# Kernel optimization log

Measured on AMD Instinct MI355X. Metric: run time of the kernel, lower is better.

The kernel has to match this reference:

```python
import jax, jax.numpy as jnp
import numpy as np
import math

D_MODEL = 512
N_HEADS = 8
D_FF = 2048
EPS = 1e-5

def _layernorm(x, g, b):
    m = jnp.mean(x, axis=-1, keepdims=True)
    v = jnp.var(x, axis=-1, keepdims=True)
    return (x - m) * jax.lax.rsqrt(v + EPS) * g + b

def setup_inputs() -> dict:
    key = jax.random.key(0)
    ks = jax.random.split(key, 8)
    d, dff = D_MODEL, D_FF
    s = lambda fan: 1.0 / math.sqrt(fan)
    return {
        "x": jax.random.normal(ks[0], (4, 2048, d), dtype=jnp.float32),
        "w_qkv": jax.random.normal(ks[1], (d, 3 * d), dtype=jnp.float32) * s(d),
        "b_qkv": jnp.zeros((3 * d,), dtype=jnp.float32),
        "w1": jax.random.normal(ks[2], (d, dff), dtype=jnp.float32) * s(d),
        "b1": jnp.zeros((dff,), dtype=jnp.float32),
        "w2": jax.random.normal(ks[3], (dff, d), dtype=jnp.float32) * s(dff),
        "b2": jnp.zeros((d,), dtype=jnp.float32),
        "g1": jnp.ones((d,), dtype=jnp.float32),
        "be1": jnp.zeros((d,), dtype=jnp.float32),
        "g2": jnp.ones((d,), dtype=jnp.float32),
        "be2": jnp.zeros((d,), dtype=jnp.float32),
    }

def reference(x, w_qkv, b_qkv, w1, b1, w2, b2, g1, be1, g2, be2):
    B, L, d = x.shape
    H = N_HEADS
    hd = d // H
    # Faithful to original: scale = 1/sqrt(hd), scores = qk / scale = qk * sqrt(hd)
    inv_scale = math.sqrt(hd)
    qkv = x @ w_qkv + b_qkv            # [B, L, 3d]
    q, k, v = jnp.split(qkv, 3, axis=-1)
    split_heads = lambda t: t.reshape(B, L, H, hd).transpose(0, 2, 1, 3)  # [B,H,L,hd]
    q, k, v = map(split_heads, (q, k, v))
    scores = jnp.einsum('bhqd,bhkd->bhqk', q, k) * inv_scale
    attn = jax.nn.softmax(scores, axis=-1)
    out = jnp.einsum('bhqk,bhkd->bhqd', attn, v)
    out = out.transpose(0, 2, 1, 3).reshape(B, L, d)
    x = _layernorm(x + out, g1, be1)
    ff = jax.nn.relu(x @ w1 + b1) @ w2 + b2
    return _layernorm(x + ff, g2, be2)
```

## Files before the change

### kernel.cpp

```cpp
#include <hip/hip_runtime.h>

typedef _Float16 f16;
typedef _Float16 f16x4 __attribute__((ext_vector_type(4)));
typedef _Float16 f16x8 __attribute__((ext_vector_type(8)));
typedef float    f32x4 __attribute__((ext_vector_type(4)));
typedef float    f32x16 __attribute__((ext_vector_type(16)));
typedef unsigned int u32x4 __attribute__((ext_vector_type(4)));

#define QK_SCALE 11.5416528f

__device__ __forceinline__ void g2l16(const void* g, void* l) {
  __builtin_amdgcn_global_load_lds(
      (__attribute__((address_space(1))) const unsigned int*)g,
      (__attribute__((address_space(3))) unsigned int*)l, 16, 0, 0);
}

__device__ __forceinline__ f32x4 mfma16(f16x8 a, f16x8 b, f32x4 c) {
  return __builtin_amdgcn_mfma_f32_16x16x32_f16(a, b, c, 0, 0, 0);
}
__device__ __forceinline__ f32x16 mfma32(f16x8 a, f16x8 b, f32x16 c) {
  return __builtin_amdgcn_mfma_f32_32x32x16_f16(a, b, c, 0, 0, 0);
}
__device__ __forceinline__ unsigned pkrtz(float a, float b) {
  auto t = __builtin_amdgcn_cvt_pkrtz(a, b);
  return *(unsigned*)&t;
}
__device__ __forceinline__ void swap32(unsigned& a, unsigned& b) {
  asm volatile("v_permlane32_swap_b32 %0, %1" : "+v"(a), "+v"(b));
}

__device__ __forceinline__ int swz64(int row, int c) { return row * 64 + ((c ^ (row & 7)) << 3); }
__device__ __forceinline__ int swz32(int row, int c) { return row * 32 + ((c ^ ((row >> 1) & 3)) << 3); }

__global__ __launch_bounds__(256) void k_split(const float* __restrict__ in,
                                               f16* __restrict__ hi, f16* __restrict__ lo, int n4) {
  int i = blockIdx.x * 256 + threadIdx.x;
  if (i >= n4) return;
  f32x4 v = ((const f32x4*)in)[i];
  f16x4 h, l;
#pragma unroll
  for (int j = 0; j < 4; ++j) {
    f16 hv = (f16)v[j];
    h[j] = hv;
    l[j] = (f16)(v[j] - (float)hv);
  }
  ((f16x4*)hi)[i] = h;
  ((f16x4*)lo)[i] = l;
}

template <bool WLO>
__global__ __launch_bounds__(256) void k_transpose_split(const float* __restrict__ in, int K, int N,
                                                         f16* __restrict__ oh, f16* __restrict__ ol) {
  __shared__ float t[32][33];
  const int tx = threadIdx.x, ty = threadIdx.y;
  const int n0 = blockIdx.x * 32, k0 = blockIdx.y * 32;
#pragma unroll
  for (int j = 0; j < 4; ++j)
    t[ty + j * 8][tx] = in[(size_t)(k0 + ty + j * 8) * N + n0 + tx];
  __syncthreads();
#pragma unroll
  for (int j = 0; j < 4; ++j) {
    float v = t[tx][ty + j * 8];
    f16 hv = (f16)v;
    size_t o = (size_t)(n0 + ty + j * 8) * K + k0 + tx;
    oh[o] = hv;
    if (WLO) ol[o] = (f16)(v - (float)hv);
  }
}

template <int EPI, bool SPLIT>
__global__ __launch_bounds__(256, SPLIT ? 2 : 3) void k_gemm(
    const f16* __restrict__ Ah, const f16* __restrict__ Al,
    const f16* __restrict__ Bh, const f16* __restrict__ Bl,
    const float* __restrict__ bias,
    float* __restrict__ outF, float* __restrict__ outF2, f16* __restrict__ outH,
    f16* __restrict__ oqh, f16* __restrict__ oql,
    f16* __restrict__ okh, f16* __restrict__ ovT,
    int M, int N, int K, int ks) {
  constexpr int NB = SPLIT ? 2 : 1;
  __shared__ f16 As[NB][128 * 32];
  __shared__ f16 Bs[NB][128 * 32];

  const int tid = threadIdx.x;
  const int bm = blockIdx.x, bn = blockIdx.y;
  const int bnc = (EPI == 3) ? (bn & 3) : bn;
  const int half = (EPI == 3) ? (bn >> 2) : 0;
  const int hoff = half * 1024;
  const int w = tid >> 6, lane = tid & 63;
  const int wr = w >> 1, wc = w & 1;
  const int lrow = lane & 15, lgrp = lane >> 4;

  const bool useLo = SPLIT && !(EPI == 0 && bn >= 4);

  f32x4 acc[4][4] = {};

  const int nkt = K >> 5;
  for (int kt = 0; kt < nkt; ++kt) {
    __syncthreads();
    const int kk = kt << 5;
#pragma unroll
    for (int c = 0; c < 2; ++c) {
      const int i = tid + (c << 8);
      const int row = i >> 2;
      const int gch = ((i & 3) ^ ((i >> 3) & 3)) << 3;
      const size_t aoff = (size_t)(bm * 128 + row) * ks + hoff + kk + gch;
      const size_t boff = (size_t)(bnc * 128 + row) * ks + hoff + kk + gch;
      g2l16(Ah + aoff, &As[0][i * 8]);
      g2l16(Bh + boff, &Bs[0][i * 8]);
      if (SPLIT)
        if (useLo) {
          g2l16(Al + aoff, &As[1][i * 8]);
          g2l16(Bl + boff, &Bs[1][i * 8]);
        }
    }
    __syncthreads();

    f16x8 a0[4], a1[4], b0[4], b1[4];
#pragma unroll
    for (int mf = 0; mf < 4; ++mf) {
      const int off = swz32(wr * 64 + mf * 16 + lrow, lgrp);
      a0[mf] = *(const f16x8*)&As[0][off];
      if (SPLIT)
        if (useLo) a1[mf] = *(const f16x8*)&As[SPLIT ? 1 : 0][off];
    }
#pragma unroll
    for (int nf = 0; nf < 4; ++nf) {
      const int off = swz32(wc * 64 + nf * 16 + lrow, lgrp);
      b0[nf] = *(const f16x8*)&Bs[0][off];
      if (SPLIT)
        if (useLo) b1[nf] = *(const f16x8*)&Bs[SPLIT ? 1 : 0][off];
    }
#pragma unroll
    for (int mf = 0; mf < 4; ++mf)
#pragma unroll
      for (int nf = 0; nf < 4; ++nf) {
        acc[mf][nf] = mfma16(a0[mf], b0[nf], acc[mf][nf]);
        if (SPLIT)
          if (useLo) {
            acc[mf][nf] = mfma16(a0[mf], b1[nf], acc[mf][nf]);
            acc[mf][nf] = mfma16(a1[mf], b0[nf], acc[mf][nf]);
          }
      }
  }

  const int rowbase = bm * 128 + wr * 64 + lgrp * 4;
  const int colbase = bnc * 128 + wc * 64 + lrow;
#pragma unroll
  for (int mf = 0; mf < 4; ++mf) {
#pragma unroll
    for (int nf = 0; nf < 4; ++nf) {
      const int gc = colbase + nf * 16;
      const float bv = (EPI == 3 && half) ? 0.f : bias[gc];
#pragma unroll
      for (int r = 0; r < 4; ++r) {
        const int gr = rowbase + mf * 16 + r;
        const float val = acc[mf][nf][r] + bv;
        if (EPI == 0) {
          const int bb = gr >> 11, tok = gr & 2047;
          const int kind = gc >> 9, hh = (gc >> 6) & 7, dd = gc & 63;
          const size_t bhp = (size_t)((bb << 3) + hh);
          const size_t qidx = (bhp * 2048 + tok) * 64 + dd;
          if (kind == 0) {
            const float sv = val * QK_SCALE;
            const f16 hv = (f16)sv;
            oqh[qidx] = hv; oql[qidx] = (f16)(sv - (float)hv);
          } else if (kind == 1) {
            okh[qidx] = (f16)val;
          } else {
            ovT[(bhp * 64 + dd) * 2048 + tok] = (f16)val;
          }
        } else if (EPI == 1) {
          outH[(size_t)gr * N + gc] = (f16)fmaxf(val, 0.f);
        } else if (EPI == 2) {
          outF[(size_t)gr * N + gc] = val;
        } else {
          float* o = half ? outF2 : outF;
          o[(size_t)gr * N + gc] = val;
        }
      }
    }
  }
}

__global__ __launch_bounds__(256, 2) void k_attn(
    const f16* __restrict__ Qh, const f16* __restrict__ Ql,
    const f16* __restrict__ Kh, const f16* __restrict__ Vt,
    f16* __restrict__ out) {
  __shared__ f16 sK[4][64 * 64], sV[4][64 * 64];

  const int tid = threadIdx.x;
  const int wg = (blockIdx.x & 7) * 64 + (blockIdx.x >> 3);
  const int bh = wg >> 4, qt = wg & 15;
  const int w = tid >> 6, lane = tid & 63;
  const int lh = lane & 31, hh = lane >> 5;

  const int qrow = qt * 128 + w * 32 + lh;
  const size_t qoff = ((size_t)bh * 2048 + qrow) * 64;
  f16x8 qh8[4], ql8[4];
#pragma unroll
  for (int d = 0; d < 4; ++d) {
    const size_t o = qoff + d * 16 + hh * 8;
    qh8[d] = *(const f16x8*)(Qh + o);
    ql8[d] = *(const f16x8*)(Ql + o);
  }

  auto stage = [&](int b, int kt) {
    const size_t koff = ((size_t)bh * 2048 + (size_t)kt * 64) * 64;
    const size_t voff = (size_t)bh * 64 * 2048 + (size_t)kt * 64;
#pragma unroll
    for (int c = 0; c < 2; ++c) {
      const int i = tid + (c << 8);
      const int row = i >> 3;
      const int gch = ((i & 7) ^ (row & 7)) << 3;
      g2l16(Kh + koff + (size_t)row * 64 + gch, &sK[b][i * 8]);
      g2l16(Vt + voff + (size_t)row * 2048 + gch, &sV[b][i * 8]);
    }
  };

  stage(0, 0);
  stage(1, 1);
  stage(2, 2);

  float m_run = -3e38f;
  float l_run = 0.f;
  f32x16 oacc[2] = {};
  const f32x16 kZero = {};
  f32x16 sA[2] = {}, sB[2] = {};

  auto qk = [&](f32x16 (&s)[2], int bi) {
    __builtin_amdgcn_s_setprio(1);
    {
      const f16x8 k0 = *(const f16x8*)&sK[bi][swz64(lh, hh)];
      const f16x8 k1 = *(const f16x8*)&sK[bi][swz64(32 + lh, hh)];
      s[0] = mfma32(k0, qh8[0], kZero);
      s[0] = mfma32(k0, ql8[0], s[0]);
      s[1] = mfma32(k1, qh8[0], kZero);
      s[1] = mfma32(k1, ql8[0], s[1]);
    }
#pragma unroll
    for (int d = 1; d < 4; ++d) {
      const f16x8 k0 = *(const f16x8*)&sK[bi][swz64(lh, d * 2 + hh)];
      const f16x8 k1 = *(const f16x8*)&sK[bi][swz64(32 + lh, d * 2 + hh)];
      s[0] = mfma32(k0, qh8[d], s[0]);
      s[0] = mfma32(k0, ql8[d], s[0]);
      s[1] = mfma32(k1, qh8[d], s[1]);
      s[1] = mfma32(k1, ql8[d], s[1]);
    }
    __builtin_amdgcn_s_setprio(0);
  };

  auto sm_pv = [&](f32x16 (&s)[2], int bi) {
    float mt = s[0][0];
#pragma unroll
    for (int r = 0; r < 16; ++r) { mt = fmaxf(mt, s[0][r]); mt = fmaxf(mt, s[1][r]); }
    mt = fmaxf(mt, __shfl_xor(mt, 32, 64));
    float mcur = m_run;
    if (!__all(mt <= mcur + 8.0f)) {
      const float mnew = fmaxf(mcur, mt);
      const float corr = __builtin_amdgcn_exp2f(mcur - mnew);
      m_run = mnew;
      l_run *= corr;
      oacc[0] = oacc[0] * corr;
      oacc[1] = oacc[1] * corr;
      mcur = mnew;
    }
    float ps = 0.f;
    unsigned pk0[8], pk1[8];
#pragma unroll
    for (int i = 0; i < 8; ++i) {
      const float a0 = __builtin_amdgcn_exp2f(s[0][2 * i] - mcur);
      const float a1 = __builtin_amdgcn_exp2f(s[0][2 * i + 1] - mcur);
      const float b0 = __builtin_amdgcn_exp2f(s[1][2 * i] - mcur);
      const float b1 = __builtin_amdgcn_exp2f(s[1][2 * i + 1] - mcur);
      ps += (a0 + a1) + (b0 + b1);
      pk0[i] = pkrtz(a0, a1);
      pk1[i] = pkrtz(b0, b1);
    }
    ps += __shfl_xor(ps, 32, 64);
    l_run += ps;

    swap32(pk0[0], pk0[2]); swap32(pk0[1], pk0[3]);
    swap32(pk0[4], pk0[6]); swap32(pk0[5], pk0[7]);
    swap32(pk1[0], pk1[2]); swap32(pk1[1], pk1[3]);
    swap32(pk1[4], pk1[6]); swap32(pk1[5], pk1[7]);

    u32x4 pbu[4];
    pbu[0] = (u32x4){pk0[0], pk0[1], pk0[2], pk0[3]};
    pbu[1] = (u32x4){pk0[4], pk0[5], pk0[6], pk0[7]};
    pbu[2] = (u32x4){pk1[0], pk1[1], pk1[2], pk1[3]};
    pbu[3] = (u32x4){pk1[4], pk1[5], pk1[6], pk1[7]};

    __builtin_amdgcn_s_setprio(1);
#pragma unroll
    for (int s2 = 0; s2 < 4; ++s2) {
      const f16x8 pb = *(const f16x8*)&pbu[s2];
#pragma unroll
      for (int db = 0; db < 2; ++db) {
        const f16x8 v = *(const f16x8*)&sV[bi][swz64(db * 32 + lh, s2 * 2 + hh)];
        oacc[db] = mfma32(v, pb, oacc[db]);
      }
    }
    __builtin_amdgcn_s_setprio(0);
  };

  auto endwait = [&](int t) {
    if (t < 29) {
      asm volatile("s_waitcnt vmcnt(4)" ::: "memory");
    } else {
      asm volatile("s_waitcnt vmcnt(0)" ::: "memory");
    }
    __builtin_amdgcn_sched_barrier(0);
    __builtin_amdgcn_s_barrier();
    __builtin_amdgcn_sched_barrier(0);
  };

  asm volatile("s_waitcnt vmcnt(4)" ::: "memory");
  __builtin_amdgcn_sched_barrier(0);
  __builtin_amdgcn_s_barrier();
  __builtin_amdgcn_sched_barrier(0);
  qk(sA, 0);

  for (int t = 0; t < 32; t += 2) {
    {
      if (t + 1 < 32) qk(sB, (t + 1) & 3);
      if (t + 3 < 32) stage((t + 3) & 3, t + 3);
      sm_pv(sA, t & 3);
      if (t + 1 < 32) endwait(t);
    }
    if (t + 1 < 32) {
      if (t + 2 < 32) qk(sA, (t + 2) & 3);
      if (t + 4 < 32) stage((t + 4) & 3, t + 4);
      sm_pv(sB, (t + 1) & 3);
      if (t + 2 < 32) endwait(t + 1);
    }
  }

  const int b = bh >> 3, hd = bh & 7;
  const float inv = 1.0f / l_run;
  const int trow = b * 2048 + qt * 128 + w * 32 + lh;
  f16* po = out + (size_t)trow * 512 + hd * 64;
#pragma unroll
  for (int db = 0; db < 2; ++db)
#pragma unroll
    for (int rq = 0; rq < 4; ++rq) {
      f16x4 o;
#pragma unroll
      for (int j = 0; j < 4; ++j) o[j] = (f16)(oacc[db][rq * 4 + j] * inv);
      *(f16x4*)(po + db * 32 + rq * 8 + hh * 4) = o;
    }
}

__global__ __launch_bounds__(256) void k_ln1(const float* __restrict__ X, const f16* __restrict__ R,
                                             const float* __restrict__ g, const float* __restrict__ be,
                                             f16* __restrict__ outH) {
  const int row = blockIdx.x * 4 + (threadIdx.x >> 6);
  const int t = threadIdx.x & 63;
  const size_t base = (size_t)row * 512 + t * 8;
  f32x4 x0 = *(const f32x4*)(X + base);
  f32x4 x1 = *(const f32x4*)(X + base + 4);
  const f16x8 r = *(const f16x8*)(R + base);
#pragma unroll
  for (int j = 0; j < 4; ++j) { x0[j] += (float)r[j]; x1[j] += (float)r[j + 4]; }
  float s = 0.f, ss = 0.f;
#pragma unroll
  for (int j = 0; j < 4; ++j) { s += x0[j] + x1[j]; ss += x0[j] * x0[j] + x1[j] * x1[j]; }
#pragma unroll
  for (int o = 32; o; o >>= 1) {
    s += __shfl_xor(s, o, 64);
    ss += __shfl_xor(ss, o, 64);
  }
  const float mean = s * (1.f / 512.f);
  const float var = ss * (1.f / 512.f) - mean * mean;
  const float rs = rsqrtf(var + 1e-5f);
  f32x4 g0 = *(const f32x4*)(g + t * 8);
  f32x4 g1v = *(const f32x4*)(g + t * 8 + 4);
  f32x4 b0 = *(const f32x4*)(be + t * 8);
  f32x4 b1 = *(const f32x4*)(be + t * 8 + 4);
  f16x8 hx;
#pragma unroll
  for (int j = 0; j < 4; ++j) {
    hx[j] = (f16)((x0[j] - mean) * rs * g0[j] + b0[j]);
    hx[j + 4] = (f16)((x1[j] - mean) * rs * g1v[j] + b1[j]);
  }
  *(f16x8*)(outH + base) = hx;
}

__global__ __launch_bounds__(256) void k_ln2(const f16* __restrict__ Xh,
                                             const float* __restrict__ R0, const float* __restrict__ R1,
                                             const float* __restrict__ g, const float* __restrict__ be,
                                             float* __restrict__ out) {
  const int row = blockIdx.x * 4 + (threadIdx.x >> 6);
  const int t = threadIdx.x & 63;
  const size_t base = (size_t)row * 512 + t * 8;
  const f16x8 xv = *(const f16x8*)(Xh + base);
  f32x4 r00 = *(const f32x4*)(R0 + base);
  f32x4 r01 = *(const f32x4*)(R0 + base + 4);
  f32x4 r10 = *(const f32x4*)(R1 + base);
  f32x4 r11 = *(const f32x4*)(R1 + base + 4);
  f32x4 x0, x1;
#pragma unroll
  for (int j = 0; j < 4; ++j) {
    x0[j] = (float)xv[j] + r00[j] + r10[j];
    x1[j] = (float)xv[j + 4] + r01[j] + r11[j];
  }
  float s = 0.f, ss = 0.f;
#pragma unroll
  for (int j = 0; j < 4; ++j) { s += x0[j] + x1[j]; ss += x0[j] * x0[j] + x1[j] * x1[j]; }
#pragma unroll
  for (int o = 32; o; o >>= 1) {
    s += __shfl_xor(s, o, 64);
    ss += __shfl_xor(ss, o, 64);
  }
  const float mean = s * (1.f / 512.f);
  const float var = ss * (1.f / 512.f) - mean * mean;
  const float rs = rsqrtf(var + 1e-5f);
  f32x4 g0 = *(const f32x4*)(g + t * 8);
  f32x4 g1v = *(const f32x4*)(g + t * 8 + 4);
  f32x4 b0 = *(const f32x4*)(be + t * 8);
  f32x4 b1 = *(const f32x4*)(be + t * 8 + 4);
  f32x4 y0 = (x0 - mean) * rs * g0 + b0;
  f32x4 y1 = (x1 - mean) * rs * g1v + b1;
  *(f32x4*)(out + base) = y0;
  *(f32x4*)(out + base + 4) = y1;
}

extern "C" void kernel_launch(void* const* d_in, const int* in_sizes, int n_in,
                              void* d_out, int out_size, void* d_ws, size_t ws_size,
                              hipStream_t stream) {
  (void)in_sizes; (void)n_in; (void)out_size;
  const float* x = (const float*)d_in[0];
  const float* w_qkv = (const float*)d_in[1];
  const float* b_qkv = (const float*)d_in[2];
  const float* w1 = (const float*)d_in[3];
  const float* b1 = (const float*)d_in[4];
  const float* w2 = (const float*)d_in[5];
  const float* b2 = (const float*)d_in[6];
  const float* g1 = (const float*)d_in[7];
  const float* be1 = (const float*)d_in[8];
  const float* g2 = (const float*)d_in[9];
  const float* be2 = (const float*)d_in[10];
  float* out = (float*)d_out;

  char* p = (char*)d_ws;
  auto take = [&](size_t bytes) {
    char* r = p;
    p += (bytes + 255) & ~(size_t)255;
    return r;
  };
  f16* xh = (f16*)take(8192ull * 512 * 2);
  f16* xl = (f16*)take(8192ull * 512 * 2);
  f16* wqkvTh = (f16*)take(1536ull * 512 * 2);
  f16* wqkvTl = (f16*)take(1536ull * 512 * 2);
  f16* w1T = (f16*)take(2048ull * 512 * 2);
  f16* w2T = (f16*)take(512ull * 2048 * 2);
  f16* qh = (f16*)take(32ull * 2048 * 64 * 2);
  f16* ql = (f16*)take(32ull * 2048 * 64 * 2);
  f16* kh = (f16*)take(32ull * 2048 * 64 * 2);
  f16* vT = (f16*)take(32ull * 64 * 2048 * 2);
  f16* attnH = (f16*)take(8192ull * 512 * 2);
  f16* x1h = (f16*)take(8192ull * 512 * 2);
  float* ffb0 = (float*)take(8192ull * 512 * 4);
  float* ffb1 = (float*)take(8192ull * 512 * 4);
  f16* hbuf = qh;

  if ((size_t)(p - (char*)d_ws) > ws_size) return;

  dim3 tb(32, 8);
  k_split<<<4096, 256, 0, stream>>>(x, xh, xl, 8192 * 512 / 4);
  k_transpose_split<true><<<dim3(1536 / 32, 512 / 32), tb, 0, stream>>>(w_qkv, 512, 1536, wqkvTh, wqkvTl);
  k_transpose_split<false><<<dim3(2048 / 32, 512 / 32), tb, 0, stream>>>(w1, 512, 2048, w1T, nullptr);
  k_transpose_split<false><<<dim3(512 / 32, 2048 / 32), tb, 0, stream>>>(w2, 2048, 512, w2T, nullptr);

  k_gemm<0, true><<<dim3(64, 12), 256, 0, stream>>>(xh, xl, wqkvTh, wqkvTl, b_qkv,
                                                    nullptr, nullptr, nullptr, qh, ql, kh, vT,
                                                    8192, 1536, 512, 512);
  k_attn<<<512, 256, 0, stream>>>(qh, ql, kh, vT, attnH);
  k_ln1<<<2048, 256, 0, stream>>>(x, attnH, g1, be1, x1h);
  k_gemm<1, false><<<dim3(64, 16), 256, 0, stream>>>(x1h, nullptr, w1T, nullptr, b1,
                                                     nullptr, nullptr, hbuf, nullptr, nullptr, nullptr, nullptr,
                                                     8192, 2048, 512, 512);
  k_gemm<3, false><<<dim3(64, 8), 256, 0, stream>>>(hbuf, nullptr, w2T, nullptr, b2,
                                                    ffb0, ffb1, nullptr, nullptr, nullptr, nullptr, nullptr,
                                                    8192, 512, 1024, 2048);
  k_ln2<<<2048, 256, 0, stream>>>(x1h, ffb0, ffb1, g2, be2, out);
}
```

Before: 179.2 us.

## Multi-buffer GEMM LDS staging, restructure attention prefetch, store FFN partials in fp16

After: 198.7 us. +10.9%, slower.

```diff
diff --git a/kernel.cpp b/kernel.cpp
--- a/kernel.cpp
+++ b/kernel.cpp
@@ -29,6 +29,14 @@
   asm volatile("v_permlane32_swap_b32 %0, %1" : "+v"(a), "+v"(b));
 }
 
+#define WAIT_BARRIER(N)                                        \
+  do {                                                         \
+    asm volatile("s_waitcnt vmcnt(" #N ")" ::: "memory");      \
+    __builtin_amdgcn_sched_barrier(0);                         \
+    __builtin_amdgcn_s_barrier();                              \
+    __builtin_amdgcn_sched_barrier(0);                         \
+  } while (0)
+
 __device__ __forceinline__ int swz64(int row, int c) { return row * 64 + ((c ^ (row & 7)) << 3); }
 __device__ __forceinline__ int swz32(int row, int c) { return row * 32 + ((c ^ ((row >> 1) & 3)) << 3); }
 
@@ -73,13 +81,14 @@
     const f16* __restrict__ Ah, const f16* __restrict__ Al,
     const f16* __restrict__ Bh, const f16* __restrict__ Bl,
     const float* __restrict__ bias,
-    float* __restrict__ outF, float* __restrict__ outF2, f16* __restrict__ outH,
+    f16* __restrict__ outH, f16* __restrict__ outH2,
     f16* __restrict__ oqh, f16* __restrict__ oql,
     f16* __restrict__ okh, f16* __restrict__ ovT,
     int M, int N, int K, int ks) {
+  constexpr int NBUF = SPLIT ? 2 : 3;
   constexpr int NB = SPLIT ? 2 : 1;
-  __shared__ f16 As[NB][128 * 32];
-  __shared__ f16 Bs[NB][128 * 32];
+  __shared__ f16 As[NBUF][NB][128 * 32];
+  __shared__ f16 Bs[NBUF][NB][128 * 32];
 
   const int tid = threadIdx.x;
   const int bm = blockIdx.x, bn = blockIdx.y;
@@ -94,9 +103,7 @@
 
   f32x4 acc[4][4] = {};
 
-  const int nkt = K >> 5;
-  for (int kt = 0; kt < nkt; ++kt) {
-    __syncthreads();
+  auto stg = [&](int bf, int kt) {
     const int kk = kt << 5;
 #pragma unroll
     for (int c = 0; c < 2; ++c) {
@@ -105,30 +112,31 @@
       const int gch = ((i & 3) ^ ((i >> 3) & 3)) << 3;
       const size_t aoff = (size_t)(bm * 128 + row) * ks + hoff + kk + gch;
       const size_t boff = (size_t)(bnc * 128 + row) * ks + hoff + kk + gch;
-      g2l16(Ah + aoff, &As[0][i * 8]);
-      g2l16(Bh + boff, &Bs[0][i * 8]);
+      g2l16(Ah + aoff, &As[bf][0][i * 8]);
+      g2l16(Bh + boff, &Bs[bf][0][i * 8]);
       if (SPLIT)
         if (useLo) {
-          g2l16(Al + aoff, &As[1][i * 8]);
-          g2l16(Bl + boff, &Bs[1][i * 8]);
+          g2l16(Al + aoff, &As[bf][1][i * 8]);
+          g2l16(Bl + boff, &Bs[bf][1][i * 8]);
         }
     }
-    __syncthreads();
-
+  };
+
+  auto compute = [&](int bf) {
     f16x8 a0[4], a1[4], b0[4], b1[4];
 #pragma unroll
     for (int mf = 0; mf < 4; ++mf) {
       const int off = swz32(wr * 64 + mf * 16 + lrow, lgrp);
-      a0[mf] = *(const f16x8*)&As[0][off];
+      a0[mf] = *(const f16x8*)&As[bf][0][off];
       if (SPLIT)
-        if (useLo) a1[mf] = *(const f16x8*)&As[SPLIT ? 1 : 0][off];
+        if (useLo) a1[mf] = *(const f16x8*)&As[bf][SPLIT ? 1 : 0][off];
     }
 #pragma unroll
     for (int nf = 0; nf < 4; ++nf) {
       const int off = swz32(wc * 64 + nf * 16 + lrow, lgrp);
-      b0[nf] = *(const f16x8*)&Bs[0][off];
+      b0[nf] = *(const f16x8*)&Bs[bf][0][off];
       if (SPLIT)
-        if (useLo) b1[nf] = *(const f16x8*)&Bs[SPLIT ? 1 : 0][off];
+        if (useLo) b1[nf] = *(const f16x8*)&Bs[bf][SPLIT ? 1 : 0][off];
     }
 #pragma unroll
     for (int mf = 0; mf < 4; ++mf)
@@ -141,6 +149,32 @@
             acc[mf][nf] = mfma16(a1[mf], b0[nf], acc[mf][nf]);
           }
       }
+  };
+
+  const int nkt = K >> 5;
+  if constexpr (!SPLIT) {
+    stg(0, 0);
+    stg(1, 1);
+    WAIT_BARRIER(4);
+    for (int kt = 0; kt < nkt; ++kt) {
+      const int cur = kt % 3;
+      const bool more2 = (kt + 2 < nkt);
+      if (more2) stg((kt + 2) % 3, kt + 2);
+      compute(cur);
+      if (kt + 1 < nkt) {
+        if (more2) WAIT_BARRIER(4);
+        else       WAIT_BARRIER(0);
+      }
+    }
+  } else {
+    stg(0, 0);
+    WAIT_BARRIER(0);
+    for (int kt = 0; kt < nkt; ++kt) {
+      const int cur = kt & 1;
+      if (kt + 1 < nkt) stg(cur ^ 1, kt + 1);
+      compute(cur);
+      if (kt + 1 < nkt) WAIT_BARRIER(0);
+    }
   }
 
   const int rowbase = bm * 128 + wr * 64 + lgrp * 4;
@@ -171,11 +205,9 @@
           }
         } else if (EPI == 1) {
           outH[(size_t)gr * N + gc] = (f16)fmaxf(val, 0.f);
-        } else if (EPI == 2) {
-          outF[(size_t)gr * N + gc] = val;
         } else {
-          float* o = half ? outF2 : outF;
-          o[(size_t)gr * N + gc] = val;
+          f16* o = half ? outH2 : outH;
+          o[(size_t)gr * N + gc] = (f16)val;
         }
       }
     }
@@ -219,7 +251,6 @@
 
   stage(0, 0);
   stage(1, 1);
-  stage(2, 2);
 
   float m_run = -3e38f;
   float l_run = 0.f;
@@ -303,35 +334,20 @@
     __builtin_amdgcn_s_setprio(0);
   };
 
-  auto endwait = [&](int t) {
-    if (t < 29) {
-      asm volatile("s_waitcnt vmcnt(4)" ::: "memory");
-    } else {
-      asm volatile("s_waitcnt vmcnt(0)" ::: "memory");
-    }
-    __builtin_amdgcn_sched_barrier(0);
-    __builtin_amdgcn_s_barrier();
-    __builtin_amdgcn_sched_barrier(0);
-  };
-
-  asm volatile("s_waitcnt vmcnt(4)" ::: "memory");
-  __builtin_amdgcn_sched_barrier(0);
-  __builtin_amdgcn_s_barrier();
-  __builtin_amdgcn_sched_barrier(0);
+  WAIT_BARRIER(0);
   qk(sA, 0);
 
   for (int t = 0; t < 32; t += 2) {
-    {
-      if (t + 1 < 32) qk(sB, (t + 1) & 3);
-      if (t + 3 < 32) stage((t + 3) & 3, t + 3);
-      sm_pv(sA, t & 3);
-      if (t + 1 < 32) endwait(t);
-    }
-    if (t + 1 < 32) {
-      if (t + 2 < 32) qk(sA, (t + 2) & 3);
-      if (t + 4 < 32) stage((t + 4) & 3, t + 4);
-      sm_pv(sB, (t + 1) & 3);
-      if (t + 2 < 32) endwait(t + 1);
+    if (t + 2 < 32) {
+      stage((t + 2) & 3, t + 2);
+      stage((t + 3) & 3, t + 3);
+    }
+    qk(sB, (t + 1) & 3);
+    sm_pv(sA, t & 3);
+    sm_pv(sB, (t + 1) & 3);
+    if (t + 2 < 32) {
+      WAIT_BARRIER(0);
+      qk(sA, (t + 2) & 3);
     }
   }
 
@@ -386,22 +402,20 @@
 }
 
 __global__ __launch_bounds__(256) void k_ln2(const f16* __restrict__ Xh,
-                                             const float* __restrict__ R0, const float* __restrict__ R1,
+                                             const f16* __restrict__ R0, const f16* __restrict__ R1,
                                              const float* __restrict__ g, const float* __restrict__ be,
                                              float* __restrict__ out) {
   const int row = blockIdx.x * 4 + (threadIdx.x >> 6);
   const int t = threadIdx.x & 63;
   const size_t base = (size_t)row * 512 + t * 8;
   const f16x8 xv = *(const f16x8*)(Xh + base);
-  f32x4 r00 = *(const f32x4*)(R0 + base);
-  f32x4 r01 = *(const f32x4*)(R0 + base + 4);
-  f32x4 r10 = *(const f32x4*)(R1 + base);
-  f32x4 r11 = *(const f32x4*)(R1 + base + 4);
+  const f16x8 r0 = *(const f16x8*)(R0 + base);
+  const f16x8 r1 = *(const f16x8*)(R1 + base);
   f32x4 x0, x1;
 #pragma unroll
   for (int j = 0; j < 4; ++j) {
-    x0[j] = (float)xv[j] + r00[j] + r10[j];
-    x1[j] = (float)xv[j + 4] + r01[j] + r11[j];
+    x0[j] = (float)xv[j] + (float)r0[j] + (float)r1[j];
+    x1[j] = (float)xv[j + 4] + (float)r0[j + 4] + (float)r1[j + 4];
   }
   float s = 0.f, ss = 0.f;
 #pragma unroll
@@ -459,8 +473,8 @@
   f16* vT = (f16*)take(32ull * 64 * 2048 * 2);
   f16* attnH = (f16*)take(8192ull * 512 * 2);
   f16* x1h = (f16*)take(8192ull * 512 * 2);
-  float* ffb0 = (float*)take(8192ull * 512 * 4);
-  float* ffb1 = (float*)take(8192ull * 512 * 4);
+  f16* ffb0 = (f16*)take(8192ull * 512 * 2);
+  f16* ffb1 = (f16*)take(8192ull * 512 * 2);
   f16* hbuf = qh;
 
   if ((size_t)(p - (char*)d_ws) > ws_size) return;
@@ -472,15 +486,15 @@
   k_transpose_split<false><<<dim3(512 / 32, 2048 / 32), tb, 0, stream>>>(w2, 2048, 512, w2T, nullptr);
 
   k_gemm<0, true><<<dim3(64, 12), 256, 0, stream>>>(xh, xl, wqkvTh, wqkvTl, b_qkv,
-                                                    nullptr, nullptr, nullptr, qh, ql, kh, vT,
+                                                    nullptr, nullptr, qh, ql, kh, vT,
                                                     8192, 1536, 512, 512);
   k_attn<<<512, 256, 0, stream>>>(qh, ql, kh, vT, attnH);
   k_ln1<<<2048, 256, 0, stream>>>(x, attnH, g1, be1, x1h);
   k_gemm<1, false><<<dim3(64, 16), 256, 0, stream>>>(x1h, nullptr, w1T, nullptr, b1,
-                                                     nullptr, nullptr, hbuf, nullptr, nullptr, nullptr, nullptr,
+                                                     hbuf, nullptr, nullptr, nullptr, nullptr, nullptr,
                                                      8192, 2048, 512, 512);
   k_gemm<3, false><<<dim3(64, 8), 256, 0, stream>>>(hbuf, nullptr, w2T, nullptr, b2,
-                                                    ffb0, ffb1, nullptr, nullptr, nullptr, nullptr, nullptr,
+                                                    ffb0, ffb1, nullptr, nullptr, nullptr, nullptr,
                                                     8192, 512, 1024, 2048);
   k_ln2<<<2048, 256, 0, stream>>>(x1h, ffb0, ffb1, g2, be2, out);
 }
```

## Split attention KV range in two with merge kernel, simplify pipeline

Applied to the files above, without the earlier changes.

After: 186.2 us. +3.9%, slower.

```diff
diff --git a/kernel.cpp b/kernel.cpp
--- a/kernel.cpp
+++ b/kernel.cpp
@@ -28,6 +28,14 @@
 __device__ __forceinline__ void swap32(unsigned& a, unsigned& b) {
   asm volatile("v_permlane32_swap_b32 %0, %1" : "+v"(a), "+v"(b));
 }
+
+#define WAIT_BARRIER(N)                                        \
+  do {                                                         \
+    asm volatile("s_waitcnt vmcnt(" #N ")" ::: "memory");      \
+    __builtin_amdgcn_sched_barrier(0);                         \
+    __builtin_amdgcn_s_barrier();                              \
+    __builtin_amdgcn_sched_barrier(0);                         \
+  } while (0)
 
 __device__ __forceinline__ int swz64(int row, int c) { return row * 64 + ((c ^ (row & 7)) << 3); }
 __device__ __forceinline__ int swz32(int row, int c) { return row * 32 + ((c ^ ((row >> 1) & 3)) << 3); }
@@ -171,8 +179,6 @@
           }
         } else if (EPI == 1) {
           outH[(size_t)gr * N + gc] = (f16)fmaxf(val, 0.f);
-        } else if (EPI == 2) {
-          outF[(size_t)gr * N + gc] = val;
         } else {
           float* o = half ? outF2 : outF;
           o[(size_t)gr * N + gc] = val;
@@ -182,15 +188,17 @@
   }
 }
 
-__global__ __launch_bounds__(256, 2) void k_attn(
+__global__ __launch_bounds__(256, 4) void k_attn(
     const f16* __restrict__ Qh, const f16* __restrict__ Ql,
     const f16* __restrict__ Kh, const f16* __restrict__ Vt,
-    f16* __restrict__ out) {
-  __shared__ f16 sK[4][64 * 64], sV[4][64 * 64];
+    f16* __restrict__ opart, float2* __restrict__ ml) {
+  __shared__ f16 sK[2][64 * 64], sV[2][64 * 64];
 
   const int tid = threadIdx.x;
-  const int wg = (blockIdx.x & 7) * 64 + (blockIdx.x >> 3);
-  const int bh = wg >> 4, qt = wg & 15;
+  const int wg = ((blockIdx.x & 7) << 7) + (blockIdx.x >> 3);
+  const int bh = wg >> 5;
+  const int qt = (wg & 31) >> 1;
+  const int half = wg & 1;
   const int w = tid >> 6, lane = tid & 63;
   const int lh = lane & 31, hh = lane >> 5;
 
@@ -204,9 +212,10 @@
     ql8[d] = *(const f16x8*)(Ql + o);
   }
 
+  const int kt0 = half * 16;
   auto stage = [&](int b, int kt) {
-    const size_t koff = ((size_t)bh * 2048 + (size_t)kt * 64) * 64;
-    const size_t voff = (size_t)bh * 64 * 2048 + (size_t)kt * 64;
+    const size_t koff = ((size_t)bh * 2048 + (size_t)(kt0 + kt) * 64) * 64;
+    const size_t voff = (size_t)bh * 64 * 2048 + (size_t)(kt0 + kt) * 64;
 #pragma unroll
     for (int c = 0; c < 2; ++c) {
       const int i = tid + (c << 8);
@@ -217,17 +226,13 @@
     }
   };
 
-  stage(0, 0);
-  stage(1, 1);
-  stage(2, 2);
-
   float m_run = -3e38f;
   float l_run = 0.f;
   f32x16 oacc[2] = {};
   const f32x16 kZero = {};
-  f32x16 sA[2] = {}, sB[2] = {};
-
-  auto qk = [&](f32x16 (&s)[2], int bi) {
+  f32x16 s[2];
+
+  auto qk = [&](int bi) {
     __builtin_amdgcn_s_setprio(1);
     {
       const f16x8 k0 = *(const f16x8*)&sK[bi][swz64(lh, hh)];
@@ -249,7 +254,7 @@
     __builtin_amdgcn_s_setprio(0);
   };
 
-  auto sm_pv = [&](f32x16 (&s)[2], int bi) {
+  auto sm_pv = [&](int bi) {
     float mt = s[0][0];
 #pragma unroll
     for (int r = 0; r < 16; ++r) { mt = fmaxf(mt, s[0][r]); mt = fmaxf(mt, s[1][r]); }
@@ -303,42 +308,20 @@
     __builtin_amdgcn_s_setprio(0);
   };
 
-  auto endwait = [&](int t) {
-    if (t < 29) {
-      asm volatile("s_waitcnt vmcnt(4)" ::: "memory");
-    } else {
-      asm volatile("s_waitcnt vmcnt(0)" ::: "memory");
-    }
-    __builtin_amdgcn_sched_barrier(0);
-    __builtin_amdgcn_s_barrier();
-    __builtin_amdgcn_sched_barrier(0);
-  };
-
-  asm volatile("s_waitcnt vmcnt(4)" ::: "memory");
-  __builtin_amdgcn_sched_barrier(0);
-  __builtin_amdgcn_s_barrier();
-  __builtin_amdgcn_sched_barrier(0);
-  qk(sA, 0);
-
-  for (int t = 0; t < 32; t += 2) {
-    {
-      if (t + 1 < 32) qk(sB, (t + 1) & 3);
-      if (t + 3 < 32) stage((t + 3) & 3, t + 3);
-      sm_pv(sA, t & 3);
-      if (t + 1 < 32) endwait(t);
-    }
-    if (t + 1 < 32) {
-      if (t + 2 < 32) qk(sA, (t + 2) & 3);
-      if (t + 4 < 32) stage((t + 4) & 3, t + 4);
-      sm_pv(sB, (t + 1) & 3);
-      if (t + 2 < 32) endwait(t + 1);
-    }
-  }
-
-  const int b = bh >> 3, hd = bh & 7;
+  stage(0, 0);
+  WAIT_BARRIER(0);
+
+  for (int kt = 0; kt < 16; ++kt) {
+    const int cur = kt & 1;
+    if (kt + 1 < 16) stage(cur ^ 1, kt + 1);
+    qk(cur);
+    sm_pv(cur);
+    if (kt + 1 < 16) WAIT_BARRIER(0);
+  }
+
   const float inv = 1.0f / l_run;
-  const int trow = b * 2048 + qt * 128 + w * 32 + lh;
-  f16* po = out + (size_t)trow * 512 + hd * 64;
+  const int trow_l = qt * 128 + w * 32 + lh;
+  const size_t pbase = ((size_t)(half * 32 + bh) * 2048 + trow_l) * 64;
 #pragma unroll
   for (int db = 0; db < 2; ++db)
 #pragma unroll
@@ -346,8 +329,37 @@
       f16x4 o;
 #pragma unroll
       for (int j = 0; j < 4; ++j) o[j] = (f16)(oacc[db][rq * 4 + j] * inv);
-      *(f16x4*)(po + db * 32 + rq * 8 + hh * 4) = o;
-    }
+      *(f16x4*)(opart + pbase + db * 32 + rq * 8 + hh * 4) = o;
+    }
+  if (hh == 0)
+    ml[(size_t)(half * 32 + bh) * 2048 + trow_l] = make_float2(m_run, l_run);
+}
+
+__global__ __launch_bounds__(256) void k_merge(const f16* __restrict__ opart,
+                                               const float2* __restrict__ ml,
+                                               f16* __restrict__ out) {
+  const int t = blockIdx.x * 256 + threadIdx.x;
+  const int base = t * 8;
+  const int trow = base >> 9;
+  const int c0 = base & 511;
+  const int b = trow >> 11, tl = trow & 2047;
+  const int hd = c0 >> 6, d0 = c0 & 63;
+  const int bh = b * 8 + hd;
+  const size_t i0 = ((size_t)bh * 2048 + tl) * 64 + d0;
+  const size_t i1 = ((size_t)(32 + bh) * 2048 + tl) * 64 + d0;
+  const f16x8 o0 = *(const f16x8*)(opart + i0);
+  const f16x8 o1 = *(const f16x8*)(opart + i1);
+  const float2 ml0 = ml[(size_t)bh * 2048 + tl];
+  const float2 ml1 = ml[(size_t)(32 + bh) * 2048 + tl];
+  const float M = fmaxf(ml0.x, ml1.x);
+  const float w0 = ml0.y * __builtin_amdgcn_exp2f(ml0.x - M);
+  const float w1 = ml1.y * __builtin_amdgcn_exp2f(ml1.x - M);
+  const float inv = 1.f / (w0 + w1);
+  const float c0f = w0 * inv, c1f = w1 * inv;
+  f16x8 r;
+#pragma unroll
+  for (int j = 0; j < 8; ++j) r[j] = (f16)(c0f * (float)o0[j] + c1f * (float)o1[j]);
+  *(f16x8*)(out + (size_t)trow * 512 + c0) = r;
 }
 
 __global__ __launch_bounds__(256) void k_ln1(const float* __restrict__ X, const f16* __restrict__ R,
@@ -461,7 +473,9 @@
   f16* x1h = (f16*)take(8192ull * 512 * 2);
   float* ffb0 = (float*)take(8192ull * 512 * 4);
   float* ffb1 = (float*)take(8192ull * 512 * 4);
+  float* mlb = (float*)take(2ull * 32 * 2048 * 8);
   f16* hbuf = qh;
+  f16* opart = (f16*)ffb0;
 
   if ((size_t)(p - (char*)d_ws) > ws_size) return;
 
@@ -474,7 +488,8 @@
   k_gemm<0, true><<<dim3(64, 12), 256, 0, stream>>>(xh, xl, wqkvTh, wqkvTl, b_qkv,
                                                     nullptr, nullptr, nullptr, qh, ql, kh, vT,
                                                     8192, 1536, 512, 512);
-  k_attn<<<512, 256, 0, stream>>>(qh, ql, kh, vT, attnH);
+  k_attn<<<1024, 256, 0, stream>>>(qh, ql, kh, vT, opart, (float2*)mlb);
+  k_merge<<<2048, 256, 0, stream>>>(opart, (const float2*)mlb, attnH);
   k_ln1<<<2048, 256, 0, stream>>>(x, attnH, g1, be1, x1h);
   k_gemm<1, false><<<dim3(64, 16), 256, 0, stream>>>(x1h, nullptr, w1T, nullptr, b1,
                                                      nullptr, nullptr, hbuf, nullptr, nullptr, nullptr, nullptr,
```
